# Performance work log

Measured on AMD Instinct MI355X. Metric: run time of the kernel, lower is better.

The kernel has to match this reference:

```python
import jax, jax.numpy as jnp
import numpy as np

DROPOUT_P = 0.0  # undefined global `dropout_p` in source; pinned to 0 (identity) for determinism


def setup_inputs() -> dict:
    key = jax.random.key(0)
    k1, k2, k3 = jax.random.split(key, 3)
    B, Lq, Lk, D = 16, 4096, 4096, 64
    return {
        "query": jax.random.normal(k1, (B, Lq, D), dtype=jnp.float32),
        "key": jax.random.normal(k2, (B, Lk, D), dtype=jnp.float32),
        "value": jax.random.normal(k3, (B, Lk, D), dtype=jnp.float32),
        "scale_factor": jnp.ones((1,), dtype=jnp.float32),
    }


def reference(query, key, value, scale_factor):
    # scores: [B, Lq, Lk] -- the large HBM-materialized intermediate
    scores = jnp.einsum("bqd,bkd->bqk", query, key) / scale_factor
    probs = jax.nn.softmax(scores, axis=-1)
    # dropout with p = DROPOUT_P = 0.0 is the identity
    out = jnp.einsum("bqk,bkd->bqd", probs, value)
    return out
```

## Files before the change

kernel.cpp:

```cpp
#include <hip/hip_runtime.h>
#include <hip/hip_fp16.h>

typedef _Float16 half2_t __attribute__((ext_vector_type(2)));
typedef _Float16 half4_t __attribute__((ext_vector_type(4)));
typedef _Float16 half8_t __attribute__((ext_vector_type(8)));
typedef float   float4_t __attribute__((ext_vector_type(4)));

static __device__ __forceinline__ half2_t cvt_pk(float a, float b) {
    return __builtin_bit_cast(half2_t, __builtin_amdgcn_cvt_pkrtz(a, b));
}
static __device__ __forceinline__ half4_t cvt_pk4(float a, float b, float c, float d) {
    half2_t lo = cvt_pk(a, b), hi = cvt_pk(c, d);
    half4_t r;
    r[0] = lo[0]; r[1] = lo[1]; r[2] = hi[0]; r[3] = hi[1];
    return r;
}
static __device__ __forceinline__ half8_t cvt_pk8(const float4& a, const float4& b) {
    half4_t lo = cvt_pk4(a.x, a.y, a.z, a.w);
    half4_t hi = cvt_pk4(b.x, b.y, b.z, b.w);
    return __builtin_shufflevector(lo, hi, 0, 1, 2, 3, 4, 5, 6, 7);
}

namespace {
constexpr int kB       = 16;
constexpr int kL       = 4096;
constexpr int kD       = 64;
constexpr int kQTile   = 128;
constexpr int kBK      = 64;
constexpr int kTiles   = kL / kBK;
constexpr int kSplit   = 2;
constexpr int kTilesHf = kTiles / kSplit;
constexpr int kTileH   = kBK * kD;
constexpr int kKStride = 72;
constexpr int kVStride = 68;
constexpr size_t kWsHalves = (size_t)kB * kTiles * kTileH;
constexpr size_t kOHalves  = (size_t)kB * kL * kD;
}


__global__ __launch_bounds__(256) void prep_kv(const float* __restrict__ K,
                                               const float* __restrict__ V,
                                               _Float16* __restrict__ Kws,
                                               _Float16* __restrict__ Vws)
{
    int blk = blockIdx.x;
    const int tid = threadIdx.x;
    if (blk < kB * kTiles) {
        const float* src = K + (size_t)blk * kTileH;
        _Float16* dst = Kws + (size_t)blk * kTileH;
#pragma unroll
        for (int i = 0; i < 2; ++i) {
            const int task = tid + 256 * i;
            const float* p = src + task * 8;
            const float4 a  = *(const float4*)p;
            const float4 b2 = *(const float4*)(p + 4);
            *(half8_t*)(dst + task * 8) = cvt_pk8(a, b2);
        }
    } else {
        blk -= kB * kTiles;
        const float* src = V + (size_t)blk * kTileH;
        _Float16* dst = Vws + (size_t)blk * kTileH;
        const int d  = tid & 63;
        const int vw = tid >> 6;
#pragma unroll
        for (int i = 0; i < 2; ++i) {
            const int c8 = vw * 2 + i;
            const int k0 = c8 * 8;
            float p[8];
#pragma unroll
            for (int j = 0; j < 8; ++j) p[j] = src[(k0 + j) * kD + d];
            half4_t lo = cvt_pk4(p[0], p[1], p[2], p[3]);
            half4_t hi = cvt_pk4(p[4], p[5], p[6], p[7]);
            *(half8_t*)(dst + (c8 * 64 + d) * 8) =
                __builtin_shufflevector(lo, hi, 0, 1, 2, 3, 4, 5, 6, 7);
        }
    }
}

__global__ __launch_bounds__(256, 2)
void fa_fwd(const float* __restrict__ Q, const _Float16* __restrict__ Kws,
            const _Float16* __restrict__ Vws, const float* __restrict__ scale_ptr,
            float* __restrict__ Out, _Float16* __restrict__ O2ws,
            float* __restrict__ Mlws)
{
    __shared__ __align__(16) _Float16 Ksh[kBK * kKStride];
    __shared__ __align__(16) _Float16 Vsh[kD * kVStride];

    const int tid  = threadIdx.x;
    const int wave = tid >> 6;
    const int lane = tid & 63;
    const int c    = lane & 15;
    const int qd   = lane >> 4;

    const int b  = blockIdx.y;
    const int hf = blockIdx.z;
    const int q0 = blockIdx.x * kQTile + wave * 32;

    const int task0 = tid, task1 = tid + 256;
    const int vd = tid & 63;
    const int vw = tid >> 6;

    const float qscale = 1.4426950408889634f / scale_ptr[0];

    const float*    Qb = Q   + (size_t)b * kL * kD;
    const _Float16* Kt = Kws + ((size_t)b * kTiles + (size_t)hf * kTilesHf) * kTileH;
    const _Float16* Vt = Vws + ((size_t)b * kTiles + (size_t)hf * kTilesHf) * kTileH;

    half8_t qfrag[2][2];
#pragma unroll
    for (int qt = 0; qt < 2; ++qt) {
        const float* qrow = Qb + (size_t)(q0 + qt * 16 + c) * kD;
#pragma unroll
        for (int dk = 0; dk < 2; ++dk) {
            const float* p = qrow + dk * 32 + qd * 8;
            half8_t h;
#pragma unroll
            for (int j = 0; j < 8; ++j) h[j] = (_Float16)(p[j] * qscale);
            qfrag[qt][dk] = h;
        }
    }

    float4_t O[2][4];
    float4_t O5[2];
#pragma unroll
    for (int qt = 0; qt < 2; ++qt) {
        O5[qt] = (float4_t)0.0f;
#pragma unroll
        for (int dt = 0; dt < 4; ++dt) O[qt][dt] = (float4_t)0.0f;
    }
    float m_run[2] = {-__builtin_inff(), -__builtin_inff()};

    const half4_t vone = {(_Float16)1.0f, (_Float16)1.0f, (_Float16)1.0f, (_Float16)1.0f};

    half8_t kp[2], vp[2];
    kp[0] = *(const half8_t*)(Kt + task0 * 8);
    kp[1] = *(const half8_t*)(Kt + task1 * 8);
    vp[0] = *(const half8_t*)(Vt + ((vw * 2 + 0) * 64 + vd) * 8);
    vp[1] = *(const half8_t*)(Vt + ((vw * 2 + 1) * 64 + vd) * 8);

    for (int t = 0; t < kTilesHf; ++t) {
        __syncthreads();

        *(half8_t*)(&Ksh[(task0 >> 3) * kKStride + (task0 & 7) * 8]) = kp[0];
        *(half8_t*)(&Ksh[(task1 >> 3) * kKStride + (task1 & 7) * 8]) = kp[1];
#pragma unroll
        for (int i = 0; i < 2; ++i) {
            const int c8 = vw * 2 + i;
            *(half4_t*)(&Vsh[vd * kVStride + c8 * 8])     =
                __builtin_shufflevector(vp[i], vp[i], 0, 1, 2, 3);
            *(half4_t*)(&Vsh[vd * kVStride + c8 * 8 + 4]) =
                __builtin_shufflevector(vp[i], vp[i], 4, 5, 6, 7);
        }
        __syncthreads();

        {
            const int nt = (t + 1) & (kTilesHf - 1);
            const _Float16* kn = Kt + (size_t)nt * kTileH;
            const _Float16* vn = Vt + (size_t)nt * kTileH;
            kp[0] = *(const half8_t*)(kn + task0 * 8);
            kp[1] = *(const half8_t*)(kn + task1 * 8);
            vp[0] = *(const half8_t*)(vn + ((vw * 2 + 0) * 64 + vd) * 8);
            vp[1] = *(const half8_t*)(vn + ((vw * 2 + 1) * 64 + vd) * 8);
        }

        half8_t kf[4][2];
#pragma unroll
        for (int kt = 0; kt < 4; ++kt)
#pragma unroll
            for (int dk = 0; dk < 2; ++dk)
                kf[kt][dk] = *(const half8_t*)(&Ksh[(kt * 16 + c) * kKStride + dk * 32 + qd * 8]);

        float4_t S[4][2];
#pragma unroll
        for (int kt = 0; kt < 4; ++kt)
#pragma unroll
            for (int qt = 0; qt < 2; ++qt) {
                float4_t acc = {-32.0f, -32.0f, -32.0f, -32.0f};
                acc = __builtin_amdgcn_mfma_f32_16x16x32_f16(kf[kt][0], qfrag[qt][0], acc, 0, 0, 0);
                acc = __builtin_amdgcn_mfma_f32_16x16x32_f16(kf[kt][1], qfrag[qt][1], acc, 0, 0, 0);
                S[kt][qt] = acc;
            }

        half4_t pf[4][2];
#pragma unroll
        for (int qt = 0; qt < 2; ++qt) {
            float tm = S[0][qt][0];
#pragma unroll
            for (int kt = 0; kt < 4; ++kt)
#pragma unroll
                for (int r = 0; r < 4; ++r) tm = fmaxf(tm, S[kt][qt][r]);
            tm = fmaxf(tm, __shfl_xor(tm, 16));
            tm = fmaxf(tm, __shfl_xor(tm, 32));

            const bool newmax = tm > m_run[qt];
            const float mn = newmax ? tm : m_run[qt];
            if (__ballot(newmax)) {
                const float alpha = __builtin_amdgcn_exp2f(m_run[qt] - mn);
                m_run[qt] = mn;
#pragma unroll
                for (int r = 0; r < 4; ++r) {
                    const float a = __shfl(alpha, qd * 4 + r);
#pragma unroll
                    for (int dt = 0; dt < 4; ++dt) O[qt][dt][r] *= a;
                    O5[qt][r] *= a;
                }
            }

#pragma unroll
            for (int kt = 0; kt < 4; ++kt) {
                const float p0 = __builtin_amdgcn_exp2f(S[kt][qt][0] - mn);
                const float p1 = __builtin_amdgcn_exp2f(S[kt][qt][1] - mn);
                const float p2 = __builtin_amdgcn_exp2f(S[kt][qt][2] - mn);
                const float p3 = __builtin_amdgcn_exp2f(S[kt][qt][3] - mn);
                pf[kt][qt] = cvt_pk4(p0, p1, p2, p3);
            }
        }

#pragma unroll
        for (int kt = 0; kt < 4; ++kt) {
#pragma unroll
            for (int dt = 0; dt < 4; ++dt) {
                const half4_t vf = *(const half4_t*)(
                    &Vsh[(dt * 16 + c) * kVStride + kt * 16 + qd * 4]);
#pragma unroll
                for (int qt = 0; qt < 2; ++qt)
                    O[qt][dt] = __builtin_amdgcn_mfma_f32_16x16x16f16(pf[kt][qt], vf, O[qt][dt], 0, 0, 0);
            }
#pragma unroll
            for (int qt = 0; qt < 2; ++qt)
                O5[qt] = __builtin_amdgcn_mfma_f32_16x16x16f16(pf[kt][qt], vone, O5[qt], 0, 0, 0);
        }
    }

#pragma unroll
    for (int qt = 0; qt < 2; ++qt)
#pragma unroll
        for (int r = 0; r < 4; ++r) {
            const float l   = O5[qt][r];
            const float inv = 1.0f / l;
            const float mrow = __shfl(m_run[qt], qd * 4 + r);
            const int qrow  = q0 + qt * 16 + qd * 4 + r;
            if (hf == 0) {
                float* op = Out + ((size_t)b * kL + qrow) * kD;
#pragma unroll
                for (int dt = 0; dt < 4; ++dt)
                    op[dt * 16 + c] = O[qt][dt][r] * inv;
            } else {
                _Float16* op = O2ws + ((size_t)b * kL + qrow) * kD;
#pragma unroll
                for (int dt = 0; dt < 4; ++dt)
                    op[dt * 16 + c] = (_Float16)(O[qt][dt][r] * inv);
            }
            if (c == 0) {
                float* mp = Mlws + (((size_t)b * kL + qrow) * 2 + hf) * 2;
                mp[0] = mrow;
                mp[1] = l;
            }
        }
}

__global__ __launch_bounds__(256)
void combine(float* __restrict__ Out, const _Float16* __restrict__ O2ws,
             const float* __restrict__ Mlws)
{
    const int t   = threadIdx.x;
    const int row = blockIdx.x * 16 + (t >> 4);
    const int d0  = (t & 15) * 4;

    const float m1 = Mlws[(size_t)row * 4 + 0];
    const float l1 = Mlws[(size_t)row * 4 + 1];
    const float m2 = Mlws[(size_t)row * 4 + 2];
    const float l2 = Mlws[(size_t)row * 4 + 3];

    const float m  = fmaxf(m1, m2);
    float w1 = l1 * exp2f(m1 - m);
    float w2 = l2 * exp2f(m2 - m);
    const float inv = 1.0f / (w1 + w2);
    w1 *= inv; w2 *= inv;

    float* op = Out + (size_t)row * kD + d0;
    const _Float16* o2 = O2ws + (size_t)row * kD + d0;
    float4 a = *(const float4*)op;
    const half4_t h = *(const half4_t*)o2;
    a.x = a.x * w1 + (float)h[0] * w2;
    a.y = a.y * w1 + (float)h[1] * w2;
    a.z = a.z * w1 + (float)h[2] * w2;
    a.w = a.w * w1 + (float)h[3] * w2;
    *(float4*)op = a;
}

extern "C" void kernel_launch(void* const* d_in, const int* in_sizes, int n_in,
                              void* d_out, int out_size, void* d_ws, size_t ws_size,
                              hipStream_t stream) {
    const float* Q = (const float*)d_in[0];
    const float* K = (const float*)d_in[1];
    const float* V = (const float*)d_in[2];
    const float* s = (const float*)d_in[3];
    float* out = (float*)d_out;
    _Float16* Kws  = (_Float16*)d_ws;
    _Float16* Vws  = Kws + kWsHalves;
    _Float16* O2ws = Vws + kWsHalves;
    float*    Mlws = (float*)(O2ws + kOHalves);

    prep_kv<<<dim3(2 * kB * kTiles), dim3(256), 0, stream>>>(K, V, Kws, Vws);
    fa_fwd<<<dim3(kL / kQTile, kB, kSplit), dim3(256), 0, stream>>>(Q, Kws, Vws, s, out, O2ws, Mlws);
    combine<<<dim3(kB * kL / 16), dim3(256), 0, stream>>>(out, O2ws, Mlws);
}
```

Baseline: 202.0 us.

## Switch attention kernel to 32x32x16 MFMA with transposed S and lazy rescale

Replaces the 16x16 MFMA tiling with 32x32x16 f16 MFMAs. S is computed transposed so each lane owns one query row, which makes the row max and sum lane-local plus one shuffle. K rows are permuted in the prep pass so the S accumulator layout feeds the PV MFMA's B operand directly, and the row sum is computed in registers instead of via an extra ones-vector MFMA. Max rescaling is skipped unless the new max exceeds the running one by 8 (in log2 units), and occupancy is raised to 3 blocks per SM. The risks are register pressure at 3 waves and precision from the lazy rescale bound.

```diff
diff --git a/kernel.cpp b/kernel.cpp
--- a/kernel.cpp
+++ b/kernel.cpp
@@ -5,6 +5,7 @@
 typedef _Float16 half4_t __attribute__((ext_vector_type(4)));
 typedef _Float16 half8_t __attribute__((ext_vector_type(8)));
 typedef float   float4_t __attribute__((ext_vector_type(4)));
+typedef float  float16_t __attribute__((ext_vector_type(16)));
 
 static __device__ __forceinline__ half2_t cvt_pk(float a, float b) {
     return __builtin_bit_cast(half2_t, __builtin_amdgcn_cvt_pkrtz(a, b));
@@ -18,6 +19,9 @@
 static __device__ __forceinline__ half8_t cvt_pk8(const float4& a, const float4& b) {
     half4_t lo = cvt_pk4(a.x, a.y, a.z, a.w);
     half4_t hi = cvt_pk4(b.x, b.y, b.z, b.w);
+    return __builtin_shufflevector(lo, hi, 0, 1, 2, 3, 4, 5, 6, 7);
+}
+static __device__ __forceinline__ half8_t join8(half4_t lo, half4_t hi) {
     return __builtin_shufflevector(lo, hi, 0, 1, 2, 3, 4, 5, 6, 7);
 }
 
@@ -32,7 +36,7 @@
 constexpr int kTilesHf = kTiles / kSplit;
 constexpr int kTileH   = kBK * kD;
 constexpr int kKStride = 72;
-constexpr int kVStride = 68;
+constexpr int kVStride = 72;
 constexpr size_t kWsHalves = (size_t)kB * kTiles * kTileH;
 constexpr size_t kOHalves  = (size_t)kB * kL * kD;
 }
@@ -51,7 +55,10 @@
 #pragma unroll
         for (int i = 0; i < 2; ++i) {
             const int task = tid + 256 * i;
-            const float* p = src + task * 8;
+            const int row  = task >> 3;
+            const int g    = task & 7;
+            const int srow = (row & ~12) | ((row & 4) << 1) | ((row & 8) >> 1);
+            const float* p = src + srow * kD + g * 8;
             const float4 a  = *(const float4*)p;
             const float4 b2 = *(const float4*)(p + 4);
             *(half8_t*)(dst + task * 8) = cvt_pk8(a, b2);
@@ -71,13 +78,12 @@
             for (int j = 0; j < 8; ++j) p[j] = src[(k0 + j) * kD + d];
             half4_t lo = cvt_pk4(p[0], p[1], p[2], p[3]);
             half4_t hi = cvt_pk4(p[4], p[5], p[6], p[7]);
-            *(half8_t*)(dst + (c8 * 64 + d) * 8) =
-                __builtin_shufflevector(lo, hi, 0, 1, 2, 3, 4, 5, 6, 7);
-        }
-    }
-}
-
-__global__ __launch_bounds__(256, 2)
+            *(half8_t*)(dst + (c8 * 64 + d) * 8) = join8(lo, hi);
+        }
+    }
+}
+
+__global__ __launch_bounds__(256, 3)
 void fa_fwd(const float* __restrict__ Q, const _Float16* __restrict__ Kws,
             const _Float16* __restrict__ Vws, const float* __restrict__ scale_ptr,
             float* __restrict__ Out, _Float16* __restrict__ O2ws,
@@ -89,8 +95,8 @@
     const int tid  = threadIdx.x;
     const int wave = tid >> 6;
     const int lane = tid & 63;
-    const int c    = lane & 15;
-    const int qd   = lane >> 4;
+    const int l31  = lane & 31;
+    const int hi   = lane >> 5;
 
     const int b  = blockIdx.y;
     const int hf = blockIdx.z;
@@ -106,31 +112,25 @@
     const _Float16* Kt = Kws + ((size_t)b * kTiles + (size_t)hf * kTilesHf) * kTileH;
     const _Float16* Vt = Vws + ((size_t)b * kTiles + (size_t)hf * kTilesHf) * kTileH;
 
-    half8_t qfrag[2][2];
-#pragma unroll
-    for (int qt = 0; qt < 2; ++qt) {
-        const float* qrow = Qb + (size_t)(q0 + qt * 16 + c) * kD;
-#pragma unroll
-        for (int dk = 0; dk < 2; ++dk) {
-            const float* p = qrow + dk * 32 + qd * 8;
+    half8_t qfrag[4];
+    {
+        const float* qrow = Qb + (size_t)(q0 + l31) * kD;
+#pragma unroll
+        for (int kd = 0; kd < 4; ++kd) {
+            const float* p = qrow + kd * 16 + hi * 8;
             half8_t h;
 #pragma unroll
             for (int j = 0; j < 8; ++j) h[j] = (_Float16)(p[j] * qscale);
-            qfrag[qt][dk] = h;
-        }
-    }
-
-    float4_t O[2][4];
-    float4_t O5[2];
-#pragma unroll
-    for (int qt = 0; qt < 2; ++qt) {
-        O5[qt] = (float4_t)0.0f;
-#pragma unroll
-        for (int dt = 0; dt < 4; ++dt) O[qt][dt] = (float4_t)0.0f;
-    }
-    float m_run[2] = {-__builtin_inff(), -__builtin_inff()};
-
-    const half4_t vone = {(_Float16)1.0f, (_Float16)1.0f, (_Float16)1.0f, (_Float16)1.0f};
+            qfrag[kd] = h;
+        }
+    }
+
+    float16_t O[2];
+    O[0] = (float16_t)0.0f;
+    O[1] = (float16_t)0.0f;
+    float m_run = -__builtin_inff();
+    float l_run = 0.0f;
+    const float16_t Zc = (float16_t)0.0f;
 
     half8_t kp[2], vp[2];
     kp[0] = *(const half8_t*)(Kt + task0 * 8);
@@ -143,14 +143,8 @@
 
         *(half8_t*)(&Ksh[(task0 >> 3) * kKStride + (task0 & 7) * 8]) = kp[0];
         *(half8_t*)(&Ksh[(task1 >> 3) * kKStride + (task1 & 7) * 8]) = kp[1];
-#pragma unroll
-        for (int i = 0; i < 2; ++i) {
-            const int c8 = vw * 2 + i;
-            *(half4_t*)(&Vsh[vd * kVStride + c8 * 8])     =
-                __builtin_shufflevector(vp[i], vp[i], 0, 1, 2, 3);
-            *(half4_t*)(&Vsh[vd * kVStride + c8 * 8 + 4]) =
-                __builtin_shufflevector(vp[i], vp[i], 4, 5, 6, 7);
-        }
+        *(half8_t*)(&Vsh[vd * kVStride + (vw * 2 + 0) * 8]) = vp[0];
+        *(half8_t*)(&Vsh[vd * kVStride + (vw * 2 + 1) * 8]) = vp[1];
         __syncthreads();
 
         {
@@ -163,100 +157,104 @@
             vp[1] = *(const half8_t*)(vn + ((vw * 2 + 1) * 64 + vd) * 8);
         }
 
-        half8_t kf[4][2];
-#pragma unroll
-        for (int kt = 0; kt < 4; ++kt)
-#pragma unroll
-            for (int dk = 0; dk < 2; ++dk)
-                kf[kt][dk] = *(const half8_t*)(&Ksh[(kt * 16 + c) * kKStride + dk * 32 + qd * 8]);
-
-        float4_t S[4][2];
-#pragma unroll
-        for (int kt = 0; kt < 4; ++kt)
-#pragma unroll
-            for (int qt = 0; qt < 2; ++qt) {
-                float4_t acc = {-32.0f, -32.0f, -32.0f, -32.0f};
-                acc = __builtin_amdgcn_mfma_f32_16x16x32_f16(kf[kt][0], qfrag[qt][0], acc, 0, 0, 0);
-                acc = __builtin_amdgcn_mfma_f32_16x16x32_f16(kf[kt][1], qfrag[qt][1], acc, 0, 0, 0);
-                S[kt][qt] = acc;
+        float16_t S0, S1;
+        {
+            half8_t kf0, kf1;
+            kf0 = *(const half8_t*)(&Ksh[(l31)      * kKStride + 0 * 16 + hi * 8]);
+            kf1 = *(const half8_t*)(&Ksh[(32 + l31) * kKStride + 0 * 16 + hi * 8]);
+            S0 = __builtin_amdgcn_mfma_f32_32x32x16_f16(kf0, qfrag[0], Zc, 0, 0, 0);
+            S1 = __builtin_amdgcn_mfma_f32_32x32x16_f16(kf1, qfrag[0], Zc, 0, 0, 0);
+#pragma unroll
+            for (int kd = 1; kd < 4; ++kd) {
+                kf0 = *(const half8_t*)(&Ksh[(l31)      * kKStride + kd * 16 + hi * 8]);
+                kf1 = *(const half8_t*)(&Ksh[(32 + l31) * kKStride + kd * 16 + hi * 8]);
+                S0 = __builtin_amdgcn_mfma_f32_32x32x16_f16(kf0, qfrag[kd], S0, 0, 0, 0);
+                S1 = __builtin_amdgcn_mfma_f32_32x32x16_f16(kf1, qfrag[kd], S1, 0, 0, 0);
             }
-
-        half4_t pf[4][2];
-#pragma unroll
-        for (int qt = 0; qt < 2; ++qt) {
-            float tm = S[0][qt][0];
-#pragma unroll
-            for (int kt = 0; kt < 4; ++kt)
-#pragma unroll
-                for (int r = 0; r < 4; ++r) tm = fmaxf(tm, S[kt][qt][r]);
-            tm = fmaxf(tm, __shfl_xor(tm, 16));
-            tm = fmaxf(tm, __shfl_xor(tm, 32));
-
-            const bool newmax = tm > m_run[qt];
-            const float mn = newmax ? tm : m_run[qt];
-            if (__ballot(newmax)) {
-                const float alpha = __builtin_amdgcn_exp2f(m_run[qt] - mn);
-                m_run[qt] = mn;
-#pragma unroll
-                for (int r = 0; r < 4; ++r) {
-                    const float a = __shfl(alpha, qd * 4 + r);
-#pragma unroll
-                    for (int dt = 0; dt < 4; ++dt) O[qt][dt][r] *= a;
-                    O5[qt][r] *= a;
-                }
+        }
+
+#define M4(v,a) fmaxf(fmaxf(v[a], v[(a)+1]), fmaxf(v[(a)+2], v[(a)+3]))
+        float pm = fmaxf(
+            fmaxf(fmaxf(M4(S0, 0), M4(S0, 4)), fmaxf(M4(S0, 8), M4(S0, 12))),
+            fmaxf(fmaxf(M4(S1, 0), M4(S1, 4)), fmaxf(M4(S1, 8), M4(S1, 12))));
+#undef M4
+        pm = fmaxf(pm, __shfl_xor(pm, 32));
+
+        const bool need = pm > m_run + 8.0f;
+        if (__ballot(need)) {
+            const float mn    = fmaxf(m_run, pm);
+            const float alpha = __builtin_amdgcn_exp2f(m_run - mn);
+            m_run = mn;
+            l_run *= alpha;
+#pragma unroll
+            for (int r = 0; r < 16; ++r) { O[0][r] *= alpha; O[1][r] *= alpha; }
+        }
+
+#pragma unroll
+        for (int r = 0; r < 16; ++r) {
+            S0[r] = __builtin_amdgcn_exp2f(S0[r] - m_run);
+            S1[r] = __builtin_amdgcn_exp2f(S1[r] - m_run);
+        }
+        half8_t pf[4];
+        pf[0] = join8(cvt_pk4(S0[0],  S0[1],  S0[2],  S0[3]),
+                      cvt_pk4(S0[4],  S0[5],  S0[6],  S0[7]));
+        pf[1] = join8(cvt_pk4(S0[8],  S0[9],  S0[10], S0[11]),
+                      cvt_pk4(S0[12], S0[13], S0[14], S0[15]));
+        pf[2] = join8(cvt_pk4(S1[0],  S1[1],  S1[2],  S1[3]),
+                      cvt_pk4(S1[4],  S1[5],  S1[6],  S1[7]));
+        pf[3] = join8(cvt_pk4(S1[8],  S1[9],  S1[10], S1[11]),
+                      cvt_pk4(S1[12], S1[13], S1[14], S1[15]));
+#define A4(v,a) ((v[a] + v[(a)+1]) + (v[(a)+2] + v[(a)+3]))
+        float lt = ((A4(S0, 0) + A4(S0, 4)) + (A4(S0, 8) + A4(S0, 12)))
+                 + ((A4(S1, 0) + A4(S1, 4)) + (A4(S1, 8) + A4(S1, 12)));
+#undef A4
+        lt += __shfl_xor(lt, 32);
+        l_run += lt;
+
+#pragma unroll
+        for (int kb = 0; kb < 4; ++kb) {
+            const half8_t vf0 = *(const half8_t*)(
+                &Vsh[(l31)      * kVStride + kb * 16 + hi * 8]);
+            const half8_t vf1 = *(const half8_t*)(
+                &Vsh[(32 + l31) * kVStride + kb * 16 + hi * 8]);
+            O[0] = __builtin_amdgcn_mfma_f32_32x32x16_f16(vf0, pf[kb], O[0], 0, 0, 0);
+            O[1] = __builtin_amdgcn_mfma_f32_32x32x16_f16(vf1, pf[kb], O[1], 0, 0, 0);
+        }
+    }
+
+    const float inv = 1.0f / l_run;
+    const int   q   = q0 + l31;
+    if (hf == 0) {
+        float* op = Out + ((size_t)b * kL + q) * kD;
+#pragma unroll
+        for (int dt = 0; dt < 2; ++dt)
+#pragma unroll
+            for (int rr = 0; rr < 4; ++rr) {
+                const int d0 = dt * 32 + rr * 8 + hi * 4;
+                float4 w;
+                w.x = O[dt][rr * 4 + 0] * inv;
+                w.y = O[dt][rr * 4 + 1] * inv;
+                w.z = O[dt][rr * 4 + 2] * inv;
+                w.w = O[dt][rr * 4 + 3] * inv;
+                *(float4*)(op + d0) = w;
             }
-
-#pragma unroll
-            for (int kt = 0; kt < 4; ++kt) {
-                const float p0 = __builtin_amdgcn_exp2f(S[kt][qt][0] - mn);
-                const float p1 = __builtin_amdgcn_exp2f(S[kt][qt][1] - mn);
-                const float p2 = __builtin_amdgcn_exp2f(S[kt][qt][2] - mn);
-                const float p3 = __builtin_amdgcn_exp2f(S[kt][qt][3] - mn);
-                pf[kt][qt] = cvt_pk4(p0, p1, p2, p3);
+    } else {
+        _Float16* op = O2ws + ((size_t)b * kL + q) * kD;
+#pragma unroll
+        for (int dt = 0; dt < 2; ++dt)
+#pragma unroll
+            for (int rr = 0; rr < 4; ++rr) {
+                const int d0 = dt * 32 + rr * 8 + hi * 4;
+                half4_t w = cvt_pk4(O[dt][rr * 4 + 0] * inv, O[dt][rr * 4 + 1] * inv,
+                                    O[dt][rr * 4 + 2] * inv, O[dt][rr * 4 + 3] * inv);
+                *(half4_t*)(op + d0) = w;
             }
-        }
-
-#pragma unroll
-        for (int kt = 0; kt < 4; ++kt) {
-#pragma unroll
-            for (int dt = 0; dt < 4; ++dt) {
-                const half4_t vf = *(const half4_t*)(
-                    &Vsh[(dt * 16 + c) * kVStride + kt * 16 + qd * 4]);
-#pragma unroll
-                for (int qt = 0; qt < 2; ++qt)
-                    O[qt][dt] = __builtin_amdgcn_mfma_f32_16x16x16f16(pf[kt][qt], vf, O[qt][dt], 0, 0, 0);
-            }
-#pragma unroll
-            for (int qt = 0; qt < 2; ++qt)
-                O5[qt] = __builtin_amdgcn_mfma_f32_16x16x16f16(pf[kt][qt], vone, O5[qt], 0, 0, 0);
-        }
-    }
-
-#pragma unroll
-    for (int qt = 0; qt < 2; ++qt)
-#pragma unroll
-        for (int r = 0; r < 4; ++r) {
-            const float l   = O5[qt][r];
-            const float inv = 1.0f / l;
-            const float mrow = __shfl(m_run[qt], qd * 4 + r);
-            const int qrow  = q0 + qt * 16 + qd * 4 + r;
-            if (hf == 0) {
-                float* op = Out + ((size_t)b * kL + qrow) * kD;
-#pragma unroll
-                for (int dt = 0; dt < 4; ++dt)
-                    op[dt * 16 + c] = O[qt][dt][r] * inv;
-            } else {
-                _Float16* op = O2ws + ((size_t)b * kL + qrow) * kD;
-#pragma unroll
-                for (int dt = 0; dt < 4; ++dt)
-                    op[dt * 16 + c] = (_Float16)(O[qt][dt][r] * inv);
-            }
-            if (c == 0) {
-                float* mp = Mlws + (((size_t)b * kL + qrow) * 2 + hf) * 2;
-                mp[0] = mrow;
-                mp[1] = l;
-            }
-        }
+    }
+    if (hi == 0) {
+        float* mp = Mlws + (((size_t)b * kL + q) * 2 + hf) * 2;
+        mp[0] = m_run;
+        mp[1] = l_run;
+    }
 }
 
 __global__ __launch_bounds__(256)
```

New measurement: 188.5 us. 6.7% less time.
